# Performance work log

Measured on AMD Instinct MI355X. Metric: run time of the kernel, lower is better.

Reference implementation:

```python
import jax, jax.numpy as jnp
import numpy as np

B, T, D, H = 4, 2048, 1024, 16
HD = D // H  # head_dim = 64
SCALE = HD ** -0.5


def setup_inputs() -> dict:
    key = jax.random.key(0)
    k1, k2, k3 = jax.random.split(key, 3)
    x = jax.random.normal(k1, (B, T, D), dtype=jnp.float32)
    # xavier-uniform-like scaling for weights
    qkv_w = jax.random.normal(k2, (3 * D, D), dtype=jnp.float32) * (2.0 / (4 * D)) ** 0.5
    out_w = jax.random.normal(k3, (D, D), dtype=jnp.float32) * (1.0 / D) ** 0.5
    out_b = jnp.zeros((D,), dtype=jnp.float32)
    return {"x": x, "qkv_w": qkv_w, "out_w": out_w, "out_b": out_b}


def reference(x, qkv_w, out_w, out_b):
    Bx, Tx, _ = x.shape
    # qkv projection (nn.Linear: x @ W^T), no bias
    qkv = jnp.einsum('btd,ed->bte', x, qkv_w)  # [B,T,3D]
    qkv = qkv.reshape(Bx, Tx, 3, H, HD).transpose(2, 0, 3, 1, 4)  # [3,B,H,T,hd]
    q, k, v = qkv[0], qkv[1], qkv[2]
    scores = jnp.einsum('bhqd,bhkd->bhqk', q, k) * SCALE  # [B,H,T,T]
    causal = jnp.triu(jnp.ones((Tx, Tx), dtype=bool), k=1)
    scores = jnp.where(causal, -jnp.inf, scores)
    weights = jax.nn.softmax(scores, axis=-1)
    out = jnp.einsum('bhqk,bhkd->bhqd', weights, v)  # [B,H,T,hd]
    out = out.transpose(0, 2, 1, 3).reshape(Bx, Tx, D)
    return jnp.einsum('btd,ed->bte', out, out_w) + out_b
```

## Files before the change

### kernel.cpp

```cpp
#include <hip/hip_runtime.h>
#include <stdint.h>


typedef __bf16 bfx8 __attribute__((ext_vector_type(8)));
typedef float f32x4 __attribute__((ext_vector_type(4)));
typedef float f32x16 __attribute__((ext_vector_type(16)));

__device__ __forceinline__ uint16_t f2b(float f) {
  uint32_t u = __float_as_uint(f);
  u += 0x7fff + ((u >> 16) & 1);
  return (uint16_t)(u >> 16);
}

__device__ __forceinline__ uint32_t cvt_pk(float lo, float hi) {
  uint32_t r;
  asm("v_cvt_pk_bf16_f32 %0, %1, %2" : "=v"(r) : "v"(lo), "v"(hi));
  return r;
}

__device__ __forceinline__ void gld16(const void* g, void* l) {
  __builtin_amdgcn_global_load_lds((const __attribute__((address_space(1))) void*)g,
                                   (__attribute__((address_space(3))) void*)l,
                                   16, 0, 0);
}

__global__ __launch_bounds__(256) void cvt_all(const float* __restrict__ x,
                                               const float* __restrict__ w1,
                                               const float* __restrict__ w2,
                                               uint16_t* __restrict__ xb,
                                               uint16_t* __restrict__ w1b,
                                               uint16_t* __restrict__ w2b) {
  int i = blockIdx.x * 256 + threadIdx.x;
  const float* in;
  uint16_t* out;
  if (i < 1048576) { in = x; out = xb; }
  else if (i < 1048576 + 393216) { in = w1; out = w1b; i -= 1048576; }
  else { in = w2; out = w2b; i -= 1048576 + 393216; }
  float4 a = ((const float4*)in)[2 * i];
  float4 b = ((const float4*)in)[2 * i + 1];
  union { uint16_t u[8]; uint4 v; } pk;
  pk.u[0] = f2b(a.x); pk.u[1] = f2b(a.y); pk.u[2] = f2b(a.z); pk.u[3] = f2b(a.w);
  pk.u[4] = f2b(b.x); pk.u[5] = f2b(b.y); pk.u[6] = f2b(b.z); pk.u[7] = f2b(b.w);
  ((uint4*)out)[i] = pk.v;
}

template <int OUTF32>
__global__ __launch_bounds__(256) void gemm_bt(const uint16_t* __restrict__ A,
                                               const uint16_t* __restrict__ B,
                                               void* __restrict__ Cout,
                                               const float* __restrict__ bias,
                                               int M, int N, int K, int nbx, int nwg) {
  __shared__ alignas(16) uint16_t As[2][128 * 32];
  __shared__ alignas(16) uint16_t Bs[2][128 * 32];

  int did = blockIdx.x;
  int wg = (did & 7) * (nwg >> 3) + (did >> 3);
  int bx = wg % nbx, by = wg / nbx;
  int m0 = by * 128, n0 = bx * 128;

  int tid = threadIdx.x;
  int lane = tid & 63, wid = tid >> 6;
  int wm = wid >> 1, wn = wid & 1;

  int rs = wid * 16 + (lane >> 2);
  int cs = (lane & 3) * 8;

  f32x4 acc[4][4] = {};

  auto stage = [&](int buf, int kt) {
    int k0 = kt * 32;
    gld16(&A[(size_t)(m0 + rs) * K + k0 + cs],      &As[buf][wid * 512]);
    gld16(&A[(size_t)(m0 + rs + 64) * K + k0 + cs], &As[buf][wid * 512 + 2048]);
    gld16(&B[(size_t)(n0 + rs) * K + k0 + cs],      &Bs[buf][wid * 512]);
    gld16(&B[(size_t)(n0 + rs + 64) * K + k0 + cs], &Bs[buf][wid * 512 + 2048]);
  };

  stage(0, 0);
  __syncthreads();

  int nk = K >> 5;
  int cur = 0;
  int ko = (lane >> 4) * 8;
  for (int kt = 0; kt < nk; ++kt) {
    if (kt + 1 < nk) stage(cur ^ 1, kt + 1);
    bfx8 a[4], b[4];
#pragma unroll
    for (int mi = 0; mi < 4; ++mi)
      a[mi] = *(const bfx8*)&As[cur][(wm * 64 + mi * 16 + (lane & 15)) * 32 + ko];
#pragma unroll
    for (int ni = 0; ni < 4; ++ni)
      b[ni] = *(const bfx8*)&Bs[cur][(wn * 64 + ni * 16 + (lane & 15)) * 32 + ko];
#pragma unroll
    for (int mi = 0; mi < 4; ++mi)
#pragma unroll
      for (int ni = 0; ni < 4; ++ni)
        acc[mi][ni] =
            __builtin_amdgcn_mfma_f32_16x16x32_bf16(a[mi], b[ni], acc[mi][ni], 0, 0, 0);
    __syncthreads();
    cur ^= 1;
  }

#pragma unroll
  for (int mi = 0; mi < 4; ++mi) {
    int row = m0 + wm * 64 + mi * 16 + ((lane >> 4) << 2);
#pragma unroll
    for (int ni = 0; ni < 4; ++ni) {
      int col = n0 + wn * 64 + ni * 16 + (lane & 15);
#pragma unroll
      for (int r = 0; r < 4; ++r) {
        float v = acc[mi][ni][r];
        if (OUTF32)
          ((float*)Cout)[(size_t)(row + r) * N + col] = v + bias[col];
        else
          ((uint16_t*)Cout)[(size_t)(row + r) * N + col] = f2b(v);
      }
    }
  }
}

__global__ __launch_bounds__(256, 2) void flash_attn(const uint16_t* __restrict__ qkv,
                                                     uint16_t* __restrict__ attnb) {
  const int T = 2048, D3 = 3072;
  const float CSC = 0.125f * 1.44269504f;
  __shared__ alignas(16) uint16_t Ks[3][64 * 64];
  __shared__ alignas(16) uint16_t Vt[3][64 * 64];

  int did = blockIdx.x;
  int bh = did & 63;
  int k = did >> 6;
  int b = bh >> 4, h = bh & 15;

  const int P1[12] = {15, 14, 13, 12,  7, 10,  9, 11,  6,  5,  4,  8};
  const int P2[12] = {-1, -1, -1, -1,  0, -1, -1, -1,  1,  2,  3, -1};
  int p1 = P1[k], p2 = P2[k];

  int tid = threadIdx.x, lane = tid & 63, wid = tid >> 6;
  int l31 = lane & 31, hi = lane >> 5;
  int swz = (lane & 7) << 3;

  size_t base = (size_t)b * T * D3;
  int hoff = h * 64;
  const uint16_t* kbase = &qkv[base + 1024 + hoff];
  const uint16_t* vbase = &qkv[base + 2048 + hoff];

  int krow = wid * 16 + (lane >> 3);
  int kc = ((lane & 7) << 3) ^ ((krow & 7) << 3);
  int vr = (tid & 31) * 2;
  int vc = (tid >> 5) * 8;

  int nparts = (p2 >= 0) ? 2 : 1;
  for (int p = 0; p < nparts; ++p) {
    int qb = (p == 0) ? p1 : p2;
    int q0 = qb << 7;
    int qw = q0 + wid * 32;
    int ntile = 2 * qb + 2;

    float mC = -1e30f, l_r = 0.f;
    f32x16 acc0 = {}, acc1 = {};
    bfx8 pf[4];
    int smax_prev = -1, vb_prev = 0;

    bfx8 qf[4];
    {
      const uint16_t* qp = &qkv[base + (size_t)(qw + l31) * D3 + hoff + 8 * hi];
#pragma unroll
      for (int h4 = 0; h4 < 4; ++h4) qf[h4] = *(const bfx8*)(qp + 16 * h4);
    }

    uint4 vA0, vA1, vB0, vB1;

    auto loadV = [&](int kv0, uint4& r0, uint4& r1) {
      r0 = *(const uint4*)&vbase[(size_t)(kv0 + vr) * D3 + vc];
      r1 = *(const uint4*)&vbase[(size_t)(kv0 + vr + 1) * D3 + vc];
    };
    auto stageK = [&](int buf, int kv0) {
      gld16(&kbase[(size_t)(kv0 + krow) * D3 + kc], &Ks[buf][wid * 1024]);
      gld16(&kbase[(size_t)(kv0 + krow + 8) * D3 + kc], &Ks[buf][wid * 1024 + 512]);
    };
    auto writeV = [&](int vb, const uint4& r0, const uint4& r1) {
      union { uint4 v; uint16_t u[8]; } x, y;
      x.v = r0; y.v = r1;
#pragma unroll
      for (int jj = 0; jj < 8; ++jj) {
        int hd = vc + jj;
        uint32_t pk = (uint32_t)x.u[jj] | ((uint32_t)y.u[jj] << 16);
        *(uint32_t*)&Vt[vb][hd * 64 + (vr ^ ((hd & 7) << 3))] = pk;
      }
    };
    auto doPV = [&]() {
      const uint16_t* vp = &Vt[vb_prev][0];
      __builtin_amdgcn_s_setprio(1);
#pragma unroll
      for (int s = 0; s < 4; ++s) {
        if (s <= smax_prev) {
          bfx8 v0 = *(const bfx8*)&vp[l31 * 64 + ((16 * s + 8 * hi) ^ swz)];
          acc0 = __builtin_amdgcn_mfma_f32_32x32x16_bf16(v0, pf[s], acc0, 0, 0, 0);
          bfx8 v1 = *(const bfx8*)&vp[(32 + l31) * 64 + ((16 * s + 8 * hi) ^ swz)];
          acc1 = __builtin_amdgcn_mfma_f32_32x32x16_bf16(v1, pf[s], acc1, 0, 0, 0);
        }
      }
      __builtin_amdgcn_s_setprio(0);
    };

    loadV(0, vA0, vA1);
    stageK(0, 0);
    writeV(0, vA0, vA1);
    loadV(64, vB0, vB1);
    stageK(1, 64);
    asm volatile("s_waitcnt vmcnt(0) lgkmcnt(0)" ::: "memory");
    __builtin_amdgcn_s_barrier();
    __builtin_amdgcn_sched_barrier(0);

    auto subiter = [&](int t, uint4& f0, uint4& f1, uint4& c0, uint4& c1) {
      int kv0 = t << 6;
      bool issue = (t + 2 < ntile);
      if (issue) {
        loadV((t + 2) << 6, f0, f1);
        stageK((t + 2) % 3, (t + 2) << 6);
      }
      bool active = (kv0 <= qw);
      int tmax = (qw > kv0) ? 2 : 1;
      f32x16 st0 = {}, st1 = {};
      if (active) {
        const uint16_t* kp = &Ks[t % 3][0];
        __builtin_amdgcn_s_setprio(1);
#pragma unroll
        for (int h4 = 0; h4 < 4; ++h4) {
          bfx8 kf0 = *(const bfx8*)&kp[l31 * 64 + ((16 * h4 + 8 * hi) ^ swz)];
          st0 = __builtin_amdgcn_mfma_f32_32x32x16_bf16(kf0, qf[h4], st0, 0, 0, 0);
          if (tmax == 2) {
            bfx8 kf1 = *(const bfx8*)&kp[(32 + l31) * 64 + ((16 * h4 + 8 * hi) ^ swz)];
            st1 = __builtin_amdgcn_mfma_f32_32x32x16_bf16(kf1, qf[h4], st1, 0, 0, 0);
          }
        }
        __builtin_amdgcn_s_setprio(0);
      }

      if (smax_prev >= 0) { doPV(); smax_prev = -1; }

      if (active) {
        int q = qw + l31;
        float mx0 = -1e30f, mx1 = -1e30f;
        if (kv0 == qw) {
#pragma unroll
          for (int r = 0; r < 16; ++r) {
            int kv = kv0 + (r & 3) + 8 * (r >> 2) + 4 * hi;
            float v = st0[r];
            if (kv > q) v = -1e30f;
            st0[r] = v;
            mx0 = fmaxf(mx0, v);
          }
        } else {
#pragma unroll
          for (int r = 0; r < 16; ++r) mx0 = fmaxf(mx0, st0[r]);
        }
        if (tmax == 2) {
          if (kv0 + 32 == qw) {
#pragma unroll
            for (int r = 0; r < 16; ++r) {
              int kv = kv0 + 32 + (r & 3) + 8 * (r >> 2) + 4 * hi;
              float v = st1[r];
              if (kv > q) v = -1e30f;
              st1[r] = v;
              mx1 = fmaxf(mx1, v);
            }
          } else {
#pragma unroll
            for (int r = 0; r < 16; ++r) mx1 = fmaxf(mx1, st1[r]);
          }
        }
        float mS = fmaxf(mx0, mx1) * CSC;
        if (!__all(mS - mC <= 8.0f)) {
          float mSp = fmaxf(mS, __shfl_xor(mS, 32));
          float mCn = fmaxf(mC, mSp);
          float fac = __builtin_amdgcn_exp2f(mC - mCn);
          mC = mCn;
          l_r *= fac;
          acc0 *= fac;
          acc1 *= fac;
        }
        float l0 = 0.f, l1 = 0.f, l2 = 0.f, l3 = 0.f;
#pragma unroll
        for (int r = 0; r < 16; r += 4) {
          float e0 = __builtin_amdgcn_exp2f(fmaf(st0[r], CSC, -mC));
          float e1 = __builtin_amdgcn_exp2f(fmaf(st0[r + 1], CSC, -mC));
          float e2 = __builtin_amdgcn_exp2f(fmaf(st0[r + 2], CSC, -mC));
          float e3 = __builtin_amdgcn_exp2f(fmaf(st0[r + 3], CSC, -mC));
          st0[r] = e0; st0[r + 1] = e1; st0[r + 2] = e2; st0[r + 3] = e3;
          l0 += e0; l1 += e1; l2 += e2; l3 += e3;
        }
        if (tmax == 2) {
#pragma unroll
          for (int r = 0; r < 16; r += 4) {
            float e0 = __builtin_amdgcn_exp2f(fmaf(st1[r], CSC, -mC));
            float e1 = __builtin_amdgcn_exp2f(fmaf(st1[r + 1], CSC, -mC));
            float e2 = __builtin_amdgcn_exp2f(fmaf(st1[r + 2], CSC, -mC));
            float e3 = __builtin_amdgcn_exp2f(fmaf(st1[r + 3], CSC, -mC));
            st1[r] = e0; st1[r + 1] = e1; st1[r + 2] = e2; st1[r + 3] = e3;
            l0 += e0; l1 += e1; l2 += e2; l3 += e3;
          }
        }
        l_r += (l0 + l1) + (l2 + l3);

        int smax = (qw + 31 - kv0) >> 4;
        if (smax > 3) smax = 3;
#pragma unroll
        for (int s = 0; s < 4; ++s) {
          if (s <= smax) {
            int pb = 8 * (s & 1);
            uint32_t W0, W1, W2, W3;
            if (s < 2) {
              W0 = cvt_pk(st0[pb + 0], st0[pb + 1]);
              W1 = cvt_pk(st0[pb + 2], st0[pb + 3]);
              W2 = cvt_pk(st0[pb + 4], st0[pb + 5]);
              W3 = cvt_pk(st0[pb + 6], st0[pb + 7]);
            } else {
              W0 = cvt_pk(st1[pb + 0], st1[pb + 1]);
              W1 = cvt_pk(st1[pb + 2], st1[pb + 3]);
              W2 = cvt_pk(st1[pb + 4], st1[pb + 5]);
              W3 = cvt_pk(st1[pb + 6], st1[pb + 7]);
            }
            auto rA = __builtin_amdgcn_permlane32_swap(W0, W2, false, false);
            auto rB = __builtin_amdgcn_permlane32_swap(W1, W3, false, false);
            union { uint32_t u[4]; bfx8 v; } pk;
            pk.u[0] = rA[0]; pk.u[1] = rB[0]; pk.u[2] = rA[1]; pk.u[3] = rB[1];
            pf[s] = pk.v;
          }
        }
        smax_prev = smax;
        vb_prev = t % 3;
      }

      if (t + 1 < ntile) writeV((t + 1) % 3, c0, c1);

      if (issue)
        asm volatile("s_waitcnt vmcnt(4) lgkmcnt(0)" ::: "memory");
      else
        asm volatile("s_waitcnt vmcnt(0) lgkmcnt(0)" ::: "memory");
      __builtin_amdgcn_s_barrier();
      __builtin_amdgcn_sched_barrier(0);
    };

    for (int t = 0; t < ntile; t += 2) {
      subiter(t, vA0, vA1, vB0, vB1);
      subiter(t + 1, vB0, vB1, vA0, vA1);
    }
    if (smax_prev >= 0) doPV();

    float l_tot = l_r + __shfl_xor(l_r, 32);
    __syncthreads();
    uint16_t* ow = ((uint16_t*)Ks) + wid * 2048;
    float rl = 1.0f / l_tot;
#pragma unroll
    for (int f = 0; f < 2; ++f) {
#pragma unroll
      for (int r = 0; r < 16; r += 2) {
        int hd = 32 * f + (r & 3) + 8 * (r >> 2) + 4 * hi;
        float v0 = (f ? acc1[r] : acc0[r]) * rl;
        float v1 = (f ? acc1[r + 1] : acc0[r + 1]) * rl;
        *(uint32_t*)&ow[l31 * 64 + (hd ^ ((l31 & 7) << 3))] = cvt_pk(v0, v1);
      }
    }
    int row = lane >> 1, cb = (lane & 1) * 32;
    int q = q0 + wid * 32 + row;
    int rs = (row & 7) << 3;
    uint16_t* dst = &attnb[(size_t)(b * T + q) * 1024 + hoff + cb];
#pragma unroll
    for (int cc = 0; cc < 4; ++cc)
      *(uint4*)&dst[cc * 8] = *(const uint4*)&ow[row * 64 + ((cb + cc * 8) ^ rs)];
    __syncthreads();
  }
}

extern "C" void kernel_launch(void* const* d_in, const int* in_sizes, int n_in,
                              void* d_out, int out_size, void* d_ws, size_t ws_size,
                              hipStream_t stream) {
  const float* x = (const float*)d_in[0];
  const float* qkv_w = (const float*)d_in[1];
  const float* out_w = (const float*)d_in[2];
  const float* out_b = (const float*)d_in[3];
  float* out = (float*)d_out;

  char* ws = (char*)d_ws;
  uint16_t* xb    = (uint16_t*)(ws);
  uint16_t* qkvb  = (uint16_t*)(ws + 16777216);
  uint16_t* attnb = (uint16_t*)(ws + 67108864);
  uint16_t* wqkvb = (uint16_t*)(ws + 83886080);
  uint16_t* wob   = (uint16_t*)(ws + 90177536);

  cvt_all<<<6144, 256, 0, stream>>>(x, qkv_w, out_w, xb, wqkvb, wob);

  gemm_bt<0><<<1536, 256, 0, stream>>>(xb, wqkvb, (void*)qkvb, nullptr,
                                       8192, 3072, 1024, 24, 1536);
  flash_attn<<<768, 256, 0, stream>>>(qkvb, attnb);
  gemm_bt<1><<<512, 256, 0, stream>>>(attnb, wob, (void*)out, out_b,
                                      8192, 1024, 1024, 8, 512);
}
```

Baseline: 197.3 us.

## Give each attention wave two 32-row query groups and pair causal blocks per workgroup

Each wave now processes 64 query rows as two 32-row groups that share every staged K and V tile, and each workgroup handles 256-row query blocks. A workgroup takes the pair (7-a, a), which replaces the old 12-entry lookup table for balancing causal work. The grid shrinks from 768 to 256 workgroups. This doubles MFMA work per LDS K/V read and halves K/V staging traffic per query row, at the cost of more registers (two accumulator sets, two Q fragment sets) and far fewer workgroups to fill the GPU.

```diff
diff --git a/kernel.cpp b/kernel.cpp
--- a/kernel.cpp
+++ b/kernel.cpp
@@ -127,12 +127,8 @@
 
   int did = blockIdx.x;
   int bh = did & 63;
-  int k = did >> 6;
+  int a = did >> 6;
   int b = bh >> 4, h = bh & 15;
-
-  const int P1[12] = {15, 14, 13, 12,  7, 10,  9, 11,  6,  5,  4,  8};
-  const int P2[12] = {-1, -1, -1, -1,  0, -1, -1, -1,  1,  2,  3, -1};
-  int p1 = P1[k], p2 = P2[k];
 
   int tid = threadIdx.x, lane = tid & 63, wid = tid >> 6;
   int l31 = lane & 31, hi = lane >> 5;
@@ -148,23 +144,27 @@
   int vr = (tid & 31) * 2;
   int vc = (tid >> 5) * 8;
 
-  int nparts = (p2 >= 0) ? 2 : 1;
-  for (int p = 0; p < nparts; ++p) {
-    int qb = (p == 0) ? p1 : p2;
-    int q0 = qb << 7;
-    int qw = q0 + wid * 32;
-    int ntile = 2 * qb + 2;
-
-    float mC = -1e30f, l_r = 0.f;
-    f32x16 acc0 = {}, acc1 = {};
-    bfx8 pf[4];
-    int smax_prev = -1, vb_prev = 0;
-
-    bfx8 qf[4];
+  for (int p = 0; p < 2; ++p) {
+    int qb = (p == 0) ? (7 - a) : a;
+    int q0 = qb << 8;
+    int qw = q0 + wid * 64;
+    int qA = qw, qB = qw + 32;
+    int ntile = 4 * qb + 4;
+
+    float mCA = -1e30f, lA = 0.f, mCB = -1e30f, lB = 0.f;
+    f32x16 accA0 = {}, accA1 = {}, accB0 = {}, accB1 = {};
+    bfx8 pfA[4], pfB[4];
+    int smaxA_p = -1, smaxB_p = -1, vb_prev = 0;
+
+    bfx8 qfA[4], qfB[4];
     {
-      const uint16_t* qp = &qkv[base + (size_t)(qw + l31) * D3 + hoff + 8 * hi];
-#pragma unroll
-      for (int h4 = 0; h4 < 4; ++h4) qf[h4] = *(const bfx8*)(qp + 16 * h4);
+      const uint16_t* qpA = &qkv[base + (size_t)(qA + l31) * D3 + hoff + 8 * hi];
+      const uint16_t* qpB = &qkv[base + (size_t)(qB + l31) * D3 + hoff + 8 * hi];
+#pragma unroll
+      for (int h4 = 0; h4 < 4; ++h4) {
+        qfA[h4] = *(const bfx8*)(qpA + 16 * h4);
+        qfB[h4] = *(const bfx8*)(qpB + 16 * h4);
+      }
     }
 
     uint4 vA0, vA1, vB0, vB1;
@@ -192,11 +192,15 @@
       __builtin_amdgcn_s_setprio(1);
 #pragma unroll
       for (int s = 0; s < 4; ++s) {
-        if (s <= smax_prev) {
+        if (s <= smaxB_p) {
           bfx8 v0 = *(const bfx8*)&vp[l31 * 64 + ((16 * s + 8 * hi) ^ swz)];
-          acc0 = __builtin_amdgcn_mfma_f32_32x32x16_bf16(v0, pf[s], acc0, 0, 0, 0);
           bfx8 v1 = *(const bfx8*)&vp[(32 + l31) * 64 + ((16 * s + 8 * hi) ^ swz)];
-          acc1 = __builtin_amdgcn_mfma_f32_32x32x16_bf16(v1, pf[s], acc1, 0, 0, 0);
+          if (s <= smaxA_p) {
+            accA0 = __builtin_amdgcn_mfma_f32_32x32x16_bf16(v0, pfA[s], accA0, 0, 0, 0);
+            accA1 = __builtin_amdgcn_mfma_f32_32x32x16_bf16(v1, pfA[s], accA1, 0, 0, 0);
+          }
+          accB0 = __builtin_amdgcn_mfma_f32_32x32x16_bf16(v0, pfB[s], accB0, 0, 0, 0);
+          accB1 = __builtin_amdgcn_mfma_f32_32x32x16_bf16(v1, pfB[s], accB1, 0, 0, 0);
         }
       }
       __builtin_amdgcn_s_setprio(0);
@@ -218,116 +222,123 @@
         loadV((t + 2) << 6, f0, f1);
         stageK((t + 2) % 3, (t + 2) << 6);
       }
-      bool active = (kv0 <= qw);
-      int tmax = (qw > kv0) ? 2 : 1;
-      f32x16 st0 = {}, st1 = {};
-      if (active) {
+      bool actA = (kv0 <= qA), actB = (kv0 <= qB);
+      int tmaxA = (qA > kv0) ? 2 : 1, tmaxB = (qB > kv0) ? 2 : 1;
+      f32x16 sA0 = {}, sA1 = {}, sB0 = {}, sB1 = {};
+
+      if (smaxB_p >= 0) { doPV(); smaxA_p = -1; smaxB_p = -1; }
+
+      if (actB) {
         const uint16_t* kp = &Ks[t % 3][0];
         __builtin_amdgcn_s_setprio(1);
 #pragma unroll
         for (int h4 = 0; h4 < 4; ++h4) {
           bfx8 kf0 = *(const bfx8*)&kp[l31 * 64 + ((16 * h4 + 8 * hi) ^ swz)];
-          st0 = __builtin_amdgcn_mfma_f32_32x32x16_bf16(kf0, qf[h4], st0, 0, 0, 0);
-          if (tmax == 2) {
+          if (actA) sA0 = __builtin_amdgcn_mfma_f32_32x32x16_bf16(kf0, qfA[h4], sA0, 0, 0, 0);
+          sB0 = __builtin_amdgcn_mfma_f32_32x32x16_bf16(kf0, qfB[h4], sB0, 0, 0, 0);
+          if (actA) {
             bfx8 kf1 = *(const bfx8*)&kp[(32 + l31) * 64 + ((16 * h4 + 8 * hi) ^ swz)];
-            st1 = __builtin_amdgcn_mfma_f32_32x32x16_bf16(kf1, qf[h4], st1, 0, 0, 0);
+            if (tmaxA == 2) sA1 = __builtin_amdgcn_mfma_f32_32x32x16_bf16(kf1, qfA[h4], sA1, 0, 0, 0);
+            sB1 = __builtin_amdgcn_mfma_f32_32x32x16_bf16(kf1, qfB[h4], sB1, 0, 0, 0);
           }
         }
         __builtin_amdgcn_s_setprio(0);
-      }
-
-      if (smax_prev >= 0) { doPV(); smax_prev = -1; }
-
-      if (active) {
-        int q = qw + l31;
-        float mx0 = -1e30f, mx1 = -1e30f;
-        if (kv0 == qw) {
-#pragma unroll
-          for (int r = 0; r < 16; ++r) {
-            int kv = kv0 + (r & 3) + 8 * (r >> 2) + 4 * hi;
-            float v = st0[r];
-            if (kv > q) v = -1e30f;
-            st0[r] = v;
-            mx0 = fmaxf(mx0, v);
-          }
-        } else {
-#pragma unroll
-          for (int r = 0; r < 16; ++r) mx0 = fmaxf(mx0, st0[r]);
-        }
-        if (tmax == 2) {
-          if (kv0 + 32 == qw) {
+
+        auto softpack = [&](f32x16& s0, f32x16& s1, int tmaxg, int qg, float& mCg,
+                            float& lg, f32x16& a0, f32x16& a1, bfx8* pfg) -> int {
+          int q = qg + l31;
+          float mx0 = -1e30f, mx1 = -1e30f;
+          if (kv0 == qg) {
 #pragma unroll
             for (int r = 0; r < 16; ++r) {
-              int kv = kv0 + 32 + (r & 3) + 8 * (r >> 2) + 4 * hi;
-              float v = st1[r];
+              int kv = kv0 + (r & 3) + 8 * (r >> 2) + 4 * hi;
+              float v = s0[r];
               if (kv > q) v = -1e30f;
-              st1[r] = v;
-              mx1 = fmaxf(mx1, v);
+              s0[r] = v;
+              mx0 = fmaxf(mx0, v);
             }
           } else {
 #pragma unroll
-            for (int r = 0; r < 16; ++r) mx1 = fmaxf(mx1, st1[r]);
-          }
-        }
-        float mS = fmaxf(mx0, mx1) * CSC;
-        if (!__all(mS - mC <= 8.0f)) {
-          float mSp = fmaxf(mS, __shfl_xor(mS, 32));
-          float mCn = fmaxf(mC, mSp);
-          float fac = __builtin_amdgcn_exp2f(mC - mCn);
-          mC = mCn;
-          l_r *= fac;
-          acc0 *= fac;
-          acc1 *= fac;
-        }
-        float l0 = 0.f, l1 = 0.f, l2 = 0.f, l3 = 0.f;
-#pragma unroll
-        for (int r = 0; r < 16; r += 4) {
-          float e0 = __builtin_amdgcn_exp2f(fmaf(st0[r], CSC, -mC));
-          float e1 = __builtin_amdgcn_exp2f(fmaf(st0[r + 1], CSC, -mC));
-          float e2 = __builtin_amdgcn_exp2f(fmaf(st0[r + 2], CSC, -mC));
-          float e3 = __builtin_amdgcn_exp2f(fmaf(st0[r + 3], CSC, -mC));
-          st0[r] = e0; st0[r + 1] = e1; st0[r + 2] = e2; st0[r + 3] = e3;
-          l0 += e0; l1 += e1; l2 += e2; l3 += e3;
-        }
-        if (tmax == 2) {
+            for (int r = 0; r < 16; ++r) mx0 = fmaxf(mx0, s0[r]);
+          }
+          if (tmaxg == 2) {
+            if (kv0 + 32 == qg) {
+#pragma unroll
+              for (int r = 0; r < 16; ++r) {
+                int kv = kv0 + 32 + (r & 3) + 8 * (r >> 2) + 4 * hi;
+                float v = s1[r];
+                if (kv > q) v = -1e30f;
+                s1[r] = v;
+                mx1 = fmaxf(mx1, v);
+              }
+            } else {
+#pragma unroll
+              for (int r = 0; r < 16; ++r) mx1 = fmaxf(mx1, s1[r]);
+            }
+          }
+          float mS = fmaxf(mx0, mx1) * CSC;
+          if (!__all(mS - mCg <= 8.0f)) {
+            float mSp = fmaxf(mS, __shfl_xor(mS, 32));
+            float mCn = fmaxf(mCg, mSp);
+            float fac = __builtin_amdgcn_exp2f(mCg - mCn);
+            mCg = mCn;
+            lg *= fac;
+            a0 *= fac;
+            a1 *= fac;
+          }
+          float l0 = 0.f, l1 = 0.f, l2 = 0.f, l3 = 0.f;
 #pragma unroll
           for (int r = 0; r < 16; r += 4) {
-            float e0 = __builtin_amdgcn_exp2f(fmaf(st1[r], CSC, -mC));
-            float e1 = __builtin_amdgcn_exp2f(fmaf(st1[r + 1], CSC, -mC));
-            float e2 = __builtin_amdgcn_exp2f(fmaf(st1[r + 2], CSC, -mC));
-            float e3 = __builtin_amdgcn_exp2f(fmaf(st1[r + 3], CSC, -mC));
-            st1[r] = e0; st1[r + 1] = e1; st1[r + 2] = e2; st1[r + 3] = e3;
+            float e0 = __builtin_amdgcn_exp2f(fmaf(s0[r], CSC, -mCg));
+            float e1 = __builtin_amdgcn_exp2f(fmaf(s0[r + 1], CSC, -mCg));
+            float e2 = __builtin_amdgcn_exp2f(fmaf(s0[r + 2], CSC, -mCg));
+            float e3 = __builtin_amdgcn_exp2f(fmaf(s0[r + 3], CSC, -mCg));
+            s0[r] = e0; s0[r + 1] = e1; s0[r + 2] = e2; s0[r + 3] = e3;
             l0 += e0; l1 += e1; l2 += e2; l3 += e3;
           }
-        }
-        l_r += (l0 + l1) + (l2 + l3);
-
-        int smax = (qw + 31 - kv0) >> 4;
-        if (smax > 3) smax = 3;
-#pragma unroll
-        for (int s = 0; s < 4; ++s) {
-          if (s <= smax) {
-            int pb = 8 * (s & 1);
-            uint32_t W0, W1, W2, W3;
-            if (s < 2) {
-              W0 = cvt_pk(st0[pb + 0], st0[pb + 1]);
-              W1 = cvt_pk(st0[pb + 2], st0[pb + 3]);
-              W2 = cvt_pk(st0[pb + 4], st0[pb + 5]);
-              W3 = cvt_pk(st0[pb + 6], st0[pb + 7]);
-            } else {
-              W0 = cvt_pk(st1[pb + 0], st1[pb + 1]);
-              W1 = cvt_pk(st1[pb + 2], st1[pb + 3]);
-              W2 = cvt_pk(st1[pb + 4], st1[pb + 5]);
-              W3 = cvt_pk(st1[pb + 6], st1[pb + 7]);
+          if (tmaxg == 2) {
+#pragma unroll
+            for (int r = 0; r < 16; r += 4) {
+              float e0 = __builtin_amdgcn_exp2f(fmaf(s1[r], CSC, -mCg));
+              float e1 = __builtin_amdgcn_exp2f(fmaf(s1[r + 1], CSC, -mCg));
+              float e2 = __builtin_amdgcn_exp2f(fmaf(s1[r + 2], CSC, -mCg));
+              float e3 = __builtin_amdgcn_exp2f(fmaf(s1[r + 3], CSC, -mCg));
+              s1[r] = e0; s1[r + 1] = e1; s1[r + 2] = e2; s1[r + 3] = e3;
+              l0 += e0; l1 += e1; l2 += e2; l3 += e3;
             }
-            auto rA = __builtin_amdgcn_permlane32_swap(W0, W2, false, false);
-            auto rB = __builtin_amdgcn_permlane32_swap(W1, W3, false, false);
-            union { uint32_t u[4]; bfx8 v; } pk;
-            pk.u[0] = rA[0]; pk.u[1] = rB[0]; pk.u[2] = rA[1]; pk.u[3] = rB[1];
-            pf[s] = pk.v;
-          }
-        }
-        smax_prev = smax;
+          }
+          lg += (l0 + l1) + (l2 + l3);
+
+          int smax = (qg + 31 - kv0) >> 4;
+          if (smax > 3) smax = 3;
+#pragma unroll
+          for (int s = 0; s < 4; ++s) {
+            if (s <= smax) {
+              int pb = 8 * (s & 1);
+              uint32_t W0, W1, W2, W3;
+              if (s < 2) {
+                W0 = cvt_pk(s0[pb + 0], s0[pb + 1]);
+                W1 = cvt_pk(s0[pb + 2], s0[pb + 3]);
+                W2 = cvt_pk(s0[pb + 4], s0[pb + 5]);
+                W3 = cvt_pk(s0[pb + 6], s0[pb + 7]);
+              } else {
+                W0 = cvt_pk(s1[pb + 0], s1[pb + 1]);
+                W1 = cvt_pk(s1[pb + 2], s1[pb + 3]);
+                W2 = cvt_pk(s1[pb + 4], s1[pb + 5]);
+                W3 = cvt_pk(s1[pb + 6], s1[pb + 7]);
+              }
+              auto rA = __builtin_amdgcn_permlane32_swap(W0, W2, false, false);
+              auto rB = __builtin_amdgcn_permlane32_swap(W1, W3, false, false);
+              union { uint32_t u[4]; bfx8 v; } pk;
+              pk.u[0] = rA[0]; pk.u[1] = rB[0]; pk.u[2] = rA[1]; pk.u[3] = rB[1];
+              pfg[s] = pk.v;
+            }
+          }
+          return smax;
+        };
+
+        if (actA) smaxA_p = softpack(sA0, sA1, tmaxA, qA, mCA, lA, accA0, accA1, pfA);
+        smaxB_p = softpack(sB0, sB1, tmaxB, qB, mCB, lB, accB0, accB1, pfB);
         vb_prev = t % 3;
       }
 
@@ -345,29 +356,40 @@
       subiter(t, vA0, vA1, vB0, vB1);
       subiter(t + 1, vB0, vB1, vA0, vA1);
     }
-    if (smax_prev >= 0) doPV();
-
-    float l_tot = l_r + __shfl_xor(l_r, 32);
+    if (smaxB_p >= 0) doPV();
+
+    float ltA = lA + __shfl_xor(lA, 32);
+    float ltB = lB + __shfl_xor(lB, 32);
     __syncthreads();
-    uint16_t* ow = ((uint16_t*)Ks) + wid * 2048;
-    float rl = 1.0f / l_tot;
-#pragma unroll
-    for (int f = 0; f < 2; ++f) {
-#pragma unroll
-      for (int r = 0; r < 16; r += 2) {
-        int hd = 32 * f + (r & 3) + 8 * (r >> 2) + 4 * hi;
-        float v0 = (f ? acc1[r] : acc0[r]) * rl;
-        float v1 = (f ? acc1[r + 1] : acc0[r + 1]) * rl;
-        *(uint32_t*)&ow[l31 * 64 + (hd ^ ((l31 & 7) << 3))] = cvt_pk(v0, v1);
+    uint16_t* ow = ((uint16_t*)Ks) + wid * 4096;
+    float rlA = 1.0f / ltA, rlB = 1.0f / ltB;
+#pragma unroll
+    for (int g = 0; g < 2; ++g) {
+      int prow = g * 32 + l31;
+      float rl = g ? rlB : rlA;
+#pragma unroll
+      for (int f = 0; f < 2; ++f) {
+#pragma unroll
+        for (int r = 0; r < 16; r += 2) {
+          int hd = 32 * f + (r & 3) + 8 * (r >> 2) + 4 * hi;
+          float v0, v1;
+          if (g == 0) { v0 = (f ? accA1[r] : accA0[r]); v1 = (f ? accA1[r + 1] : accA0[r + 1]); }
+          else        { v0 = (f ? accB1[r] : accB0[r]); v1 = (f ? accB1[r + 1] : accB0[r + 1]); }
+          *(uint32_t*)&ow[prow * 64 + (hd ^ ((l31 & 7) << 3))] = cvt_pk(v0 * rl, v1 * rl);
+        }
       }
     }
-    int row = lane >> 1, cb = (lane & 1) * 32;
-    int q = q0 + wid * 32 + row;
-    int rs = (row & 7) << 3;
-    uint16_t* dst = &attnb[(size_t)(b * T + q) * 1024 + hoff + cb];
-#pragma unroll
-    for (int cc = 0; cc < 4; ++cc)
-      *(uint4*)&dst[cc * 8] = *(const uint4*)&ow[row * 64 + ((cb + cc * 8) ^ rs)];
+#pragma unroll
+    for (int f2 = 0; f2 < 2; ++f2) {
+      int row = f2 * 32 + (lane >> 1);
+      int cb = (lane & 1) * 32;
+      int q = q0 + wid * 64 + row;
+      int rs = (row & 7) << 3;
+      uint16_t* dst = &attnb[(size_t)(b * T + q) * 1024 + hoff + cb];
+#pragma unroll
+      for (int cc = 0; cc < 4; ++cc)
+        *(uint4*)&dst[cc * 8] = *(const uint4*)&ow[row * 64 + ((cb + cc * 8) ^ rs)];
+    }
     __syncthreads();
   }
 }
@@ -392,7 +414,7 @@
 
   gemm_bt<0><<<1536, 256, 0, stream>>>(xb, wqkvb, (void*)qkvb, nullptr,
                                        8192, 3072, 1024, 24, 1536);
-  flash_attn<<<768, 256, 0, stream>>>(qkvb, attnb);
+  flash_attn<<<256, 256, 0, stream>>>(qkvb, attnb);
   gemm_bt<1><<<512, 256, 0, stream>>>(attnb, wob, (void*)out, out_b,
                                       8192, 1024, 1024, 8, 512);
 }
```

After: 237.3 us. 1.2x slower.
